# Performance work log

Measured on AMD Instinct MI355X. Metric: run time of the kernel, lower is better.

The kernel has to match this reference:

```python
import jax, jax.numpy as jnp
import numpy as np

B, S, HID = 1, 4096, 2048
NH, NKV, HD = 16, 4, 128
BLK, LOCAL, GNB, STRIDE = 64, 4, 2, 4
ROT = 64  # head_dim * rope_partial_rotary_factor(0.5), already even
SCALE = HD ** -0.5
NEG = -1e9


def _block_select(nb):
    """Static local+global key-block selection per query block (mirrors _select_key_blocks)."""
    sels = []
    for bi in range(nb):
        local = list(range(max(0, bi - LOCAL + 1), bi + 1))
        gc = list(range(0, bi + 1, STRIDE))
        if len(gc) > GNB:
            gc = gc[-GNB:]
        if 0 not in gc:
            gc = [0] + gc
        idx = sorted(set(local + gc))
        sels.append([i for i in idx if 0 <= i < nb and i <= bi])
    m = max(len(s) for s in sels)
    idx = np.zeros((nb, m), np.int32)
    valid = np.zeros((nb, m), bool)
    for i, s in enumerate(sels):
        idx[i, :len(s)] = s
        valid[i, :len(s)] = True
    return jnp.asarray(idx), jnp.asarray(valid)


def _rot_half(x):
    h = x.shape[-1] // 2
    return jnp.concatenate([-x[..., h:], x[..., :h]], axis=-1)


def setup_inputs() -> dict:
    key = jax.random.key(0)
    ks = jax.random.split(key, 8)
    w = lambda k, shp: (jax.random.normal(k, shp, jnp.float32) * 0.02)
    return {
        "hidden": jax.random.normal(ks[0], (B, S, HID), jnp.float32),
        "cos": jax.random.uniform(ks[1], (B, S, ROT), jnp.float32, -1.0, 1.0),
        "sin": jax.random.uniform(ks[2], (B, S, ROT), jnp.float32, -1.0, 1.0),
        "Wq": w(ks[3], (HID, NH * HD)),
        "Wk": w(ks[4], (HID, NKV * HD)),
        "Wv": w(ks[5], (HID, NKV * HD)),
        "Wo": w(ks[6], (NH * HD, HID)),
        "attn_mask": jnp.ones((B, S), jnp.float32),
    }


def reference(hidden, cos, sin, Wq, Wk, Wv, Wo, attn_mask):
    b_, s_, _ = hidden.shape
    q = (hidden @ Wq).reshape(b_, s_, NH, HD).transpose(0, 2, 1, 3)   # [B,H,S,d]
    k = (hidden @ Wk).reshape(b_, s_, NKV, HD).transpose(0, 2, 1, 3)  # [B,Hkv,S,d]
    v = (hidden @ Wv).reshape(b_, s_, NKV, HD).transpose(0, 2, 1, 3)

    # partial RoPE on first ROT channels
    c = cos[:, None, :, :]
    sn = sin[:, None, :, :]
    q1, q2 = q[..., :ROT], q[..., ROT:]
    k1, k2 = k[..., :ROT], k[..., ROT:]
    q = jnp.concatenate([q1 * c + _rot_half(q1) * sn, q2], axis=-1)
    k = jnp.concatenate([k1 * c + _rot_half(k1) * sn, k2], axis=-1)

    # repeat_kv (GQA expand: each kv head repeated contiguously)
    rep = NH // NKV
    k = jnp.repeat(k, rep, axis=1)
    v = jnp.repeat(v, rep, axis=1)

    nb = s_ // BLK  # S chosen divisible by BLK (pad_len == 0)
    qb = q.reshape(b_, NH, nb, BLK, HD)
    kb = k.reshape(b_, NH, nb, BLK, HD)
    vb = v.reshape(b_, NH, nb, BLK, HD)

    idx, valid = _block_select(nb)  # [nb, M]
    m = idx.shape[1]
    ksel = kb[:, :, idx]  # [B,H,nb,M,BLK,d]
    vsel = vb[:, :, idx]

    scores = jnp.einsum('bhnqd,bhnmkd->bhnqmk',
                        qb.astype(jnp.float32), ksel.astype(jnp.float32)) * SCALE
    # key-validity (padding) mask, additive as in original
    key_valid = attn_mask.reshape(b_, nb, BLK)
    kvm = key_valid[:, idx]  # [B,nb,M,BLK]
    scores = scores + (1.0 - kvm[:, None, :, None, :, :]) * NEG
    # invalid (padded) selected slots
    scores = jnp.where(valid[None, None, :, None, :, None], scores, NEG)
    # intra-block causal mask on the diagonal block
    intra = jnp.triu(jnp.ones((BLK, BLK), bool), 1)                    # [q,k]
    same = idx == jnp.arange(nb)[:, None]                              # [nb,M]
    diag = same[:, None, :, None] & intra[None, :, None, :]            # [nb,q,M,k]
    scores = jnp.where(diag[None, None], NEG, scores)

    probs = jax.nn.softmax(scores.reshape(b_, NH, nb, BLK, m * BLK), axis=-1)
    vflat = vsel.reshape(b_, NH, nb, m * BLK, HD)
    out = jnp.einsum('bhnqe,bhned->bhnqd', probs.astype(v.dtype), vflat)
    out = out.reshape(b_, NH, s_, HD).transpose(0, 2, 1, 3).reshape(b_, s_, NH * HD)
    return out @ Wo
```

## Files before the change

### kernel.cpp

```cpp
#include <hip/hip_runtime.h>
#include <hip/hip_bf16.h>


typedef short short8 __attribute__((ext_vector_type(8)));
typedef float f32x4  __attribute__((ext_vector_type(4)));

#define NEGV   (-1.0e9f)
#define SCALE  (0.08838834764831845f)

__device__ __forceinline__ void gload16(const void* g, void* l) {
  __builtin_amdgcn_global_load_lds(
      (const __attribute__((address_space(1))) unsigned int*)g,
      (__attribute__((address_space(3))) unsigned int*)l, 16, 0, 0);
}

__device__ __forceinline__ float bf2f(short s) {
  union { unsigned u; float f; } c;
  c.u = ((unsigned)(unsigned short)s) << 16;
  return c.f;
}

__device__ __forceinline__ short f2bf_s(float f) {
  __hip_bfloat16 b = __float2bfloat16(f);
  short s;
  __builtin_memcpy(&s, &b, 2);
  return s;
}

__global__ void conv_hidden(const float* __restrict__ H, __hip_bfloat16* __restrict__ X) {
  size_t t = (size_t)blockIdx.x * 256 + threadIdx.x;
  float4 v = *(const float4*)(H + t * 4);
  __hip_bfloat16* o = X + t * 4;
  o[0] = __float2bfloat16(v.x); o[1] = __float2bfloat16(v.y);
  o[2] = __float2bfloat16(v.z); o[3] = __float2bfloat16(v.w);
}

__global__ void transpose_f32_to_bf16(const float* __restrict__ src,
                                      __hip_bfloat16* __restrict__ dst,
                                      int R, int C) {
  __shared__ __hip_bfloat16 tile[64][73];
  int r0 = blockIdx.x * 64, c0 = blockIdx.y * 64;
  int c = threadIdx.x & 63, rq = threadIdx.x >> 6;
#pragma unroll
  for (int i = 0; i < 16; ++i) {
    int r = i * 4 + rq;
    tile[r][c] = __float2bfloat16(src[(size_t)(r0 + r) * C + c0 + c]);
  }
  __syncthreads();
#pragma unroll
  for (int i = 0; i < 16; ++i) {
    int cc = i * 4 + rq;
    dst[(size_t)(c0 + cc) * R + r0 + c] = tile[c][cc];
  }
}

__global__ void transpose_v(const __hip_bfloat16* __restrict__ Vb,
                            __hip_bfloat16* __restrict__ Vt) {
  __shared__ __hip_bfloat16 tile[64][73];
  int s0 = blockIdx.x * 64, c0 = blockIdx.y * 64;
  int c = threadIdx.x & 63, rq = threadIdx.x >> 6;
#pragma unroll
  for (int i = 0; i < 16; ++i) {
    int r = i * 4 + rq;
    tile[r][c] = Vb[(size_t)(s0 + r) * 512 + c0 + c];
  }
  __syncthreads();
#pragma unroll
  for (int i = 0; i < 16; ++i) {
    int cc = i * 4 + rq;
    Vt[(size_t)(c0 + cc) * 4096 + s0 + c] = tile[c][cc];
  }
}

__global__ void rope_inplace(const float* __restrict__ cosb, const float* __restrict__ sinb,
                             __hip_bfloat16* __restrict__ Qb, __hip_bfloat16* __restrict__ Kb) {
  int t = blockIdx.x * 256 + threadIdx.x;
  __hip_bfloat16* p;
  int s;
  if (t < 262144) {
    s = t >> 6;
    int rem = t & 63;
    p = Qb + (size_t)s * 2048 + (rem >> 2) * 128 + (rem & 3) * 8;
  } else {
    int tk = t - 262144;
    s = tk >> 4;
    int rem = tk & 15;
    p = Kb + (size_t)s * 512 + (rem >> 2) * 128 + (rem & 3) * 8;
  }
  const int g8 = (t & 3) * 8;
  const float* cp = cosb + (size_t)s * 64 + g8;
  const float* sp = sinb + (size_t)s * 64 + g8;
  short8 a = *(const short8*)p;
  short8 b = *(const short8*)(p + 32);
  float ca[8], sa[8], cb[8], sb[8];
  *(float4*)&ca[0] = *(const float4*)cp;        *(float4*)&ca[4] = *(const float4*)(cp + 4);
  *(float4*)&cb[0] = *(const float4*)(cp + 32); *(float4*)&cb[4] = *(const float4*)(cp + 36);
  *(float4*)&sa[0] = *(const float4*)sp;        *(float4*)&sa[4] = *(const float4*)(sp + 4);
  *(float4*)&sb[0] = *(const float4*)(sp + 32); *(float4*)&sb[4] = *(const float4*)(sp + 36);
  short8 oa, ob;
#pragma unroll
  for (int i = 0; i < 8; ++i) {
    float av = bf2f(a[i]), bv = bf2f(b[i]);
    oa[i] = f2bf_s(av * ca[i] - bv * sa[i]);
    ob[i] = f2bf_s(bv * cb[i] + av * sb[i]);
  }
  *(short8*)p = oa;
  *(short8*)(p + 32) = ob;
}

__global__ __launch_bounds__(512) void gemm_qkv256(
    const __hip_bfloat16* __restrict__ A, const __hip_bfloat16* __restrict__ Bt,
    __hip_bfloat16* __restrict__ Qb, __hip_bfloat16* __restrict__ Kb,
    __hip_bfloat16* __restrict__ Vb) {
  const int K = 2048;
  const int tid = threadIdx.x;
  const int wave = tid >> 6, lane = tid & 63;
  const int l15 = lane & 15, lg = lane >> 4;
  const int bm = blockIdx.x, bn = blockIdx.y;
  const int wm = wave >> 2, wn = wave & 3;

  __shared__ __hip_bfloat16 lds[2][32768];

  f32x4 acc[8][4] = {};
  const int lrow = lane >> 3;
  const int lslot = lane & 7;
  const size_t abase = (size_t)bm * 256 * K;
  const size_t bbase = (size_t)bn * 256 * K;
  const int r3 = l15 & 7;

#define STAGE_TILE(buf, k0)                                                        \
  do {                                                                             \
    _Pragma("unroll")                                                              \
    for (int c = 0; c < 4; ++c) {                                                  \
      int seg = c * 8 + wave;                                                      \
      int row = seg * 8 + lrow;                                                    \
      int col = (lslot ^ (row & 7)) * 8;                                           \
      gload16(A + abase + (size_t)row * K + (k0) + col, &lds[buf][seg * 512]);     \
      gload16(Bt + bbase + (size_t)row * K + (k0) + col, &lds[buf][16384 + seg * 512]); \
    }                                                                              \
  } while (0)

  STAGE_TILE(0, 0);

  for (int t = 0; t < 32; ++t) {
    asm volatile("s_waitcnt vmcnt(0)" ::: "memory");
    __builtin_amdgcn_s_barrier();
    __builtin_amdgcn_sched_barrier(0);
    if (t + 1 < 32) {
      const int nb = (t + 1) & 1;
      if (nb) STAGE_TILE(1, (t + 1) * 64); else STAGE_TILE(0, (t + 1) * 64);
    }
    const __hip_bfloat16* As_ = lds[t & 1];
    const __hip_bfloat16* Bs_ = lds[t & 1] + 16384;
#pragma unroll
    for (int kk = 0; kk < 2; ++kk) {
      const int slot = (kk * 4 + lg) ^ r3;
      short8 bf[4];
#pragma unroll
      for (int ni = 0; ni < 4; ++ni)
        bf[ni] = *(const short8*)&Bs_[(wn * 64 + ni * 16 + l15) * 64 + slot * 8];
#pragma unroll
      for (int mh = 0; mh < 2; ++mh) {
        short8 af[4];
#pragma unroll
        for (int mi = 0; mi < 4; ++mi)
          af[mi] = *(const short8*)&As_[(wm * 128 + mh * 64 + mi * 16 + l15) * 64 + slot * 8];
        __builtin_amdgcn_s_setprio(1);
#pragma unroll
        for (int mi = 0; mi < 4; ++mi)
#pragma unroll
          for (int ni = 0; ni < 4; ++ni)
            acc[mh * 4 + mi][ni] =
                __builtin_amdgcn_mfma_f32_16x16x32_bf16(af[mi], bf[ni], acc[mh * 4 + mi][ni], 0, 0, 0);
        __builtin_amdgcn_s_setprio(0);
      }
    }
  }
#undef STAGE_TILE

  __hip_bfloat16* dst; int ldc, coff;
  if (bn < 8)       { dst = Qb; ldc = 2048; coff = bn * 256; }
  else if (bn < 10) { dst = Kb; ldc = 512;  coff = bn * 256 - 2048; }
  else              { dst = Vb; ldc = 512;  coff = bn * 256 - 2560; }
#pragma unroll
  for (int m8 = 0; m8 < 8; ++m8)
#pragma unroll
    for (int ni = 0; ni < 4; ++ni) {
      int row = bm * 256 + wm * 128 + m8 * 16 + lg * 4;
      int col = coff + wn * 64 + ni * 16 + l15;
#pragma unroll
      for (int r = 0; r < 4; ++r)
        dst[(size_t)(row + r) * ldc + col] = __float2bfloat16(acc[m8][ni][r]);
    }
}

__global__ __launch_bounds__(256) void gemm_bt(
    const __hip_bfloat16* __restrict__ A, const __hip_bfloat16* __restrict__ Bt,
    float* __restrict__ C, int M, int N, int K) {
  const int tid = threadIdx.x;
  const int wave = tid >> 6, lane = tid & 63;
  const int l15 = lane & 15, lg = lane >> 4;
  const int bm = blockIdx.x, bn = blockIdx.y;
  const int wm = wave >> 1, wn = wave & 1;

  __shared__ __hip_bfloat16 As[128 * 64];
  __shared__ __hip_bfloat16 Bs[128 * 64];

  f32x4 acc[4][4] = {};
  const int lrow = lane >> 3;
  const int lslot = lane & 7;
  const int scol = (lslot ^ lrow) * 8;
  const size_t abase = (size_t)bm * 128 * K;
  const size_t bbase = (size_t)bn * 128 * K;
  const int r3 = l15 & 7;

  for (int k0 = 0; k0 < K; k0 += 64) {
#pragma unroll
    for (int i = 0; i < 4; ++i) {
      int seg = i * 4 + wave;
      int row = seg * 8 + lrow;
      gload16(A + abase + (size_t)row * K + k0 + scol, &As[seg * 512]);
      gload16(Bt + bbase + (size_t)row * K + k0 + scol, &Bs[seg * 512]);
    }
    __syncthreads();
#pragma unroll
    for (int ks = 0; ks < 2; ++ks) {
      const int slot = (ks * 4 + lg) ^ r3;
      short8 af[4], bf[4];
#pragma unroll
      for (int mi = 0; mi < 4; ++mi)
        af[mi] = *(const short8*)&As[(wm * 64 + mi * 16 + l15) * 64 + slot * 8];
#pragma unroll
      for (int ni = 0; ni < 4; ++ni)
        bf[ni] = *(const short8*)&Bs[(wn * 64 + ni * 16 + l15) * 64 + slot * 8];
#pragma unroll
      for (int mi = 0; mi < 4; ++mi)
#pragma unroll
        for (int ni = 0; ni < 4; ++ni)
          acc[mi][ni] = __builtin_amdgcn_mfma_f32_16x16x32_bf16(af[mi], bf[ni], acc[mi][ni], 0, 0, 0);
    }
    __syncthreads();
  }
#pragma unroll
  for (int mi = 0; mi < 4; ++mi)
#pragma unroll
    for (int ni = 0; ni < 4; ++ni) {
      int row = bm * 128 + wm * 64 + mi * 16 + lg * 4;
      int col = bn * 128 + wn * 64 + ni * 16 + l15;
#pragma unroll
      for (int r = 0; r < 4; ++r)
        C[(size_t)(row + r) * N + col] = acc[mi][ni][r];
    }
}

__global__ __launch_bounds__(256, 2) void attn_kernel(
    const __hip_bfloat16* __restrict__ Qb,
    const __hip_bfloat16* __restrict__ Kb,
    const __hip_bfloat16* __restrict__ Vt,
    const float* __restrict__ amask,
    __hip_bfloat16* __restrict__ AO)
{
  const int bid = blockIdx.x;
  const int h = bid & 15;
  const int bi = bid >> 4;
  const int kvh = h >> 2;
  const int tid = threadIdx.x;
  const int wave = tid >> 6, lane = tid & 63;
  const int l15 = lane & 15, lg = lane >> 4;

  int sel[6]; int nsel = 0;
  {
    int gtop = bi >> 2;
    for (int j = 0; j <= bi; ++j) {
      bool pick = (j == 0) || (j >= bi - 3) || (((j & 3) == 0) && ((j >> 2) >= gtop - 1));
      if (pick && nsel < 6) sel[nsel++] = j;
    }
  }

  __shared__ __hip_bfloat16 kvs[128 * 72];
  __shared__ __hip_bfloat16 Pb[64 * 72];

  short8 qf[4];
  {
    const __hip_bfloat16* qbase =
        Qb + (size_t)(bi * 64 + wave * 16 + l15) * 2048 + h * 128 + lg * 8;
#pragma unroll
    for (int ks = 0; ks < 4; ++ks) qf[ks] = *(const short8*)(qbase + ks * 32);
  }

  f32x4 sc[6][4] = {};
#pragma unroll
  for (int j = 0; j < 6; ++j) {
    if (j < nsel) {
      int kb = sel[j];
#pragma unroll
      for (int i = 0; i < 4; ++i) {
        int e = (i * 256 + tid) * 8;
        int r = e >> 7, c = e & 127;
        short8 v = *(const short8*)(Kb + (size_t)(kb * 64 + r) * 512 + kvh * 128 + c);
        *(short8*)&kvs[r * 136 + c] = v;
      }
      __syncthreads();
#pragma unroll
      for (int nf = 0; nf < 4; ++nf)
#pragma unroll
        for (int ks = 0; ks < 4; ++ks) {
          short8 bfr = *(const short8*)&kvs[(nf * 16 + l15) * 136 + ks * 32 + lg * 8];
          sc[j][nf] = __builtin_amdgcn_mfma_f32_16x16x32_bf16(qf[ks], bfr, sc[j][nf], 0, 0, 0);
        }
      __syncthreads();
    }
  }

  float rowmax[4] = {-3.0e38f, -3.0e38f, -3.0e38f, -3.0e38f};
#pragma unroll
  for (int j = 0; j < 6; ++j) {
    if (j >= nsel) continue;
    int kb = sel[j];
#pragma unroll
    for (int nf = 0; nf < 4; ++nf) {
      int keyg = kb * 64 + nf * 16 + l15;
      float mterm = (1.0f - amask[keyg]) * NEGV;
      int keyl = nf * 16 + l15;
#pragma unroll
      for (int r = 0; r < 4; ++r) {
        float s = sc[j][nf][r] * SCALE + mterm;
        if (kb == bi) {
          int qrow = wave * 16 + lg * 4 + r;
          if (keyl > qrow) s = NEGV;
        }
        sc[j][nf][r] = s;
        rowmax[r] = fmaxf(rowmax[r], s);
      }
    }
  }
#pragma unroll
  for (int r = 0; r < 4; ++r) {
    float v = rowmax[r];
    v = fmaxf(v, __shfl_xor(v, 1)); v = fmaxf(v, __shfl_xor(v, 2));
    v = fmaxf(v, __shfl_xor(v, 4)); v = fmaxf(v, __shfl_xor(v, 8));
    rowmax[r] = v;
  }
  float rinv[4] = {0.f, 0.f, 0.f, 0.f};
#pragma unroll
  for (int j = 0; j < 6; ++j) {
    if (j >= nsel) continue;
#pragma unroll
    for (int nf = 0; nf < 4; ++nf)
#pragma unroll
      for (int r = 0; r < 4; ++r) {
        float p = __expf(sc[j][nf][r] - rowmax[r]);
        sc[j][nf][r] = p;
        rinv[r] += p;
      }
  }
#pragma unroll
  for (int r = 0; r < 4; ++r) {
    float v = rinv[r];
    v += __shfl_xor(v, 1); v += __shfl_xor(v, 2);
    v += __shfl_xor(v, 4); v += __shfl_xor(v, 8);
    rinv[r] = 1.0f / v;
  }

  f32x4 oacc[8] = {};
#pragma unroll
  for (int j = 0; j < 6; ++j) {
    if (j < nsel) {
      int kb = sel[j];
#pragma unroll
      for (int nf = 0; nf < 4; ++nf)
#pragma unroll
        for (int r = 0; r < 4; ++r) {
          int qrow = wave * 16 + lg * 4 + r;
          Pb[qrow * 72 + nf * 16 + l15] = __float2bfloat16(sc[j][nf][r] * rinv[r]);
        }
#pragma unroll
      for (int i = 0; i < 4; ++i) {
        int e = (i * 256 + tid) * 8;
        int d = e >> 6, c = e & 63;
        short8 v = *(const short8*)(Vt + (size_t)(kvh * 128 + d) * 4096 + kb * 64 + c);
        *(short8*)&kvs[d * 72 + c] = v;
      }
      __syncthreads();
#pragma unroll
      for (int ks = 0; ks < 2; ++ks) {
        short8 pa = *(const short8*)&Pb[(wave * 16 + l15) * 72 + ks * 32 + lg * 8];
#pragma unroll
        for (int df = 0; df < 8; ++df) {
          short8 vb = *(const short8*)&kvs[(df * 16 + l15) * 72 + ks * 32 + lg * 8];
          oacc[df] = __builtin_amdgcn_mfma_f32_16x16x32_bf16(pa, vb, oacc[df], 0, 0, 0);
        }
      }
      __syncthreads();
    }
  }

#pragma unroll
  for (int df = 0; df < 8; ++df)
#pragma unroll
    for (int r = 0; r < 4; ++r) {
      int qrow = bi * 64 + wave * 16 + lg * 4 + r;
      AO[(size_t)qrow * 2048 + h * 128 + df * 16 + l15] = __float2bfloat16(oacc[df][r]);
    }
}

extern "C" void kernel_launch(void* const* d_in, const int* in_sizes, int n_in,
                              void* d_out, int out_size, void* d_ws, size_t ws_size,
                              hipStream_t stream) {
  const float* hidden = (const float*)d_in[0];
  const float* cosb   = (const float*)d_in[1];
  const float* sinb   = (const float*)d_in[2];
  const float* Wq     = (const float*)d_in[3];
  const float* Wk     = (const float*)d_in[4];
  const float* Wv     = (const float*)d_in[5];
  const float* Wo     = (const float*)d_in[6];
  const float* amask  = (const float*)d_in[7];

  char* ws = (char*)d_ws;
  __hip_bfloat16* Xb   = (__hip_bfloat16*)(ws);
  __hip_bfloat16* Wt   = (__hip_bfloat16*)(ws + 16777216);
  __hip_bfloat16* Wot  = (__hip_bfloat16*)(ws + 29360128);
  __hip_bfloat16* Qb   = (__hip_bfloat16*)(ws + 37748736);
  __hip_bfloat16* Kb   = (__hip_bfloat16*)(ws + 54525952);
  __hip_bfloat16* Vb   = (__hip_bfloat16*)(ws + 58720256);
  __hip_bfloat16* Vt   = (__hip_bfloat16*)(ws + 62914560);
  __hip_bfloat16* AO   = Xb;

  conv_hidden<<<8192, 256, 0, stream>>>(hidden, Xb);
  transpose_f32_to_bf16<<<dim3(32, 32), 256, 0, stream>>>(Wq, Wt, 2048, 2048);
  transpose_f32_to_bf16<<<dim3(32, 8),  256, 0, stream>>>(Wk, Wt + (size_t)2048 * 2048, 2048, 512);
  transpose_f32_to_bf16<<<dim3(32, 8),  256, 0, stream>>>(Wv, Wt + (size_t)2560 * 2048, 2048, 512);
  transpose_f32_to_bf16<<<dim3(32, 32), 256, 0, stream>>>(Wo, Wot, 2048, 2048);

  gemm_qkv256<<<dim3(16, 12), 512, 0, stream>>>(Xb, Wt, Qb, Kb, Vb);

  rope_inplace<<<1280, 256, 0, stream>>>(cosb, sinb, Qb, Kb);
  transpose_v<<<dim3(64, 8), 256, 0, stream>>>(Vb, Vt);

  attn_kernel<<<1024, 256, 0, stream>>>(Qb, Kb, Vt, amask, AO);

  gemm_bt<<<dim3(32, 16), 256, 0, stream>>>(AO, Wot, (float*)d_out, 4096, 2048, 2048);
}
```

Before: 174.8 us.

## Restructure QKV GEMM into eight-phase pipelined schedule with split half-tile loads

The QKV projection GEMM main loop is rewritten so each k-step runs four phases. In each phase a quarter of the A fragments is read from LDS and a half-tile of the next A or the B after that is issued as global-to-LDS loads, with barriers and partial vmcnt waits in between. B is prefetched two steps ahead and A one step ahead, which replaces the single full wait-and-barrier per iteration. This aims to spread memory traffic across the MFMA work and hide load latency. It adds more barriers per iteration, and a launch-bounds hint of two blocks per CU may constrain registers.

```diff
diff --git a/kernel.cpp b/kernel.cpp
--- a/kernel.cpp
+++ b/kernel.cpp
@@ -108,7 +108,7 @@
   *(short8*)(p + 32) = ob;
 }
 
-__global__ __launch_bounds__(512) void gemm_qkv256(
+__global__ __launch_bounds__(512, 2) void gemm_qkv8p(
     const __hip_bfloat16* __restrict__ A, const __hip_bfloat16* __restrict__ Bt,
     __hip_bfloat16* __restrict__ Qb, __hip_bfloat16* __restrict__ Kb,
     __hip_bfloat16* __restrict__ Vb) {
@@ -119,64 +119,90 @@
   const int bm = blockIdx.x, bn = blockIdx.y;
   const int wm = wave >> 2, wn = wave & 3;
 
-  __shared__ __hip_bfloat16 lds[2][32768];
+  __shared__ __hip_bfloat16 lds[65536];
 
   f32x4 acc[8][4] = {};
-  const int lrow = lane >> 3;
-  const int lslot = lane & 7;
+  const int srow = lane >> 3;
+  const int sslot = lane & 7;
+  const int scol = (sslot ^ srow) * 8;
   const size_t abase = (size_t)bm * 256 * K;
   const size_t bbase = (size_t)bn * 256 * K;
   const int r3 = l15 & 7;
 
-#define STAGE_TILE(buf, k0)                                                        \
-  do {                                                                             \
-    _Pragma("unroll")                                                              \
-    for (int c = 0; c < 4; ++c) {                                                  \
-      int seg = c * 8 + wave;                                                      \
-      int row = seg * 8 + lrow;                                                    \
-      int col = (lslot ^ (row & 7)) * 8;                                           \
-      gload16(A + abase + (size_t)row * K + (k0) + col, &lds[buf][seg * 512]);     \
-      gload16(Bt + bbase + (size_t)row * K + (k0) + col, &lds[buf][16384 + seg * 512]); \
-    }                                                                              \
+#define STAGE_HALF(SRC, SBASE, HALF, KO, LBASE)                                  \
+  do {                                                                           \
+    _Pragma("unroll")                                                            \
+    for (int l = 0; l < 2; ++l) {                                                \
+      int chunk = l * 8 + wave;                                                  \
+      int row = chunk * 8 + srow;                                                \
+      gload16(SRC + (SBASE) + (size_t)((HALF) * 128 + row) * K + (KO) + scol,    \
+              &lds[(LBASE) + chunk * 512]);                                      \
+    }                                                                            \
   } while (0)
 
-  STAGE_TILE(0, 0);
+  STAGE_HALF(Bt, bbase, 0, 0, 16384);
+  STAGE_HALF(Bt, bbase, 1, 0, 16384 + 8192);
+  STAGE_HALF(A, abase, 0, 0, 0);
+  STAGE_HALF(A, abase, 1, 0, 8192);
+  STAGE_HALF(Bt, bbase, 0, 64, 32768 + 16384);
+  STAGE_HALF(Bt, bbase, 1, 64, 32768 + 16384 + 8192);
+  asm volatile("s_waitcnt vmcnt(4)" ::: "memory");
+  __builtin_amdgcn_sched_barrier(0);
+  __builtin_amdgcn_s_barrier();
 
   for (int t = 0; t < 32; ++t) {
-    asm volatile("s_waitcnt vmcnt(0)" ::: "memory");
-    __builtin_amdgcn_s_barrier();
-    __builtin_amdgcn_sched_barrier(0);
-    if (t + 1 < 32) {
-      const int nb = (t + 1) & 1;
-      if (nb) STAGE_TILE(1, (t + 1) * 64); else STAGE_TILE(0, (t + 1) * 64);
-    }
-    const __hip_bfloat16* As_ = lds[t & 1];
-    const __hip_bfloat16* Bs_ = lds[t & 1] + 16384;
-#pragma unroll
-    for (int kk = 0; kk < 2; ++kk) {
-      const int slot = (kk * 4 + lg) ^ r3;
-      short8 bf[4];
-#pragma unroll
-      for (int ni = 0; ni < 4; ++ni)
-        bf[ni] = *(const short8*)&Bs_[(wn * 64 + ni * 16 + l15) * 64 + slot * 8];
-#pragma unroll
-      for (int mh = 0; mh < 2; ++mh) {
-        short8 af[4];
-#pragma unroll
-        for (int mi = 0; mi < 4; ++mi)
-          af[mi] = *(const short8*)&As_[(wm * 128 + mh * 64 + mi * 16 + l15) * 64 + slot * 8];
-        __builtin_amdgcn_s_setprio(1);
-#pragma unroll
-        for (int mi = 0; mi < 4; ++mi)
+    const int buf = (t & 1) * 32768;
+    const int nbuf = buf ^ 32768;
+    const int bA = buf + wm * 8192;
+    const int bB = buf + 16384 + (wn >> 1) * 8192;
+    short8 bfr[4][2];
+#pragma unroll
+    for (int q = 0; q < 4; ++q) {
+      if (q == 0) {
+#pragma unroll
+        for (int ni = 0; ni < 4; ++ni)
+#pragma unroll
+          for (int ks = 0; ks < 2; ++ks) {
+            int row = (wn & 1) * 64 + ni * 16 + l15;
+            int slot = (ks * 4 + lg) ^ r3;
+            bfr[ni][ks] = *(const short8*)&lds[bB + row * 64 + slot * 8];
+          }
+      }
+      short8 af[2][2];
+#pragma unroll
+      for (int m2 = 0; m2 < 2; ++m2)
+#pragma unroll
+        for (int ks = 0; ks < 2; ++ks) {
+          int row = (q * 2 + m2) * 16 + l15;
+          int slot = (ks * 4 + lg) ^ r3;
+          af[m2][ks] = *(const short8*)&lds[bA + row * 64 + slot * 8];
+        }
+      if (q == 0)      { if (t + 1 < 32) STAGE_HALF(A, abase, 0, (t + 1) * 64, nbuf); }
+      else if (q == 1) { if (t + 1 < 32) STAGE_HALF(A, abase, 1, (t + 1) * 64, nbuf + 8192); }
+      else if (q == 2) { if (t + 2 < 32) STAGE_HALF(Bt, bbase, 0, (t + 2) * 64, buf + 16384); }
+      else {
+        if (t + 2 < 32) STAGE_HALF(Bt, bbase, 1, (t + 2) * 64, buf + 16384 + 8192);
+        if (t < 30) asm volatile("s_waitcnt vmcnt(4)" ::: "memory");
+        else        asm volatile("s_waitcnt vmcnt(0)" ::: "memory");
+        __builtin_amdgcn_sched_barrier(0);
+      }
+      __builtin_amdgcn_s_barrier();
+      asm volatile("s_waitcnt lgkmcnt(0)" ::: "memory");
+      __builtin_amdgcn_sched_barrier(0);
+      __builtin_amdgcn_s_setprio(1);
+#pragma unroll
+      for (int ks = 0; ks < 2; ++ks)
+#pragma unroll
+        for (int m2 = 0; m2 < 2; ++m2)
 #pragma unroll
           for (int ni = 0; ni < 4; ++ni)
-            acc[mh * 4 + mi][ni] =
-                __builtin_amdgcn_mfma_f32_16x16x32_bf16(af[mi], bf[ni], acc[mh * 4 + mi][ni], 0, 0, 0);
-        __builtin_amdgcn_s_setprio(0);
-      }
-    }
-  }
-#undef STAGE_TILE
+            acc[q * 2 + m2][ni] = __builtin_amdgcn_mfma_f32_16x16x32_bf16(
+                af[m2][ks], bfr[ni][ks], acc[q * 2 + m2][ni], 0, 0, 0);
+      __builtin_amdgcn_s_setprio(0);
+      __builtin_amdgcn_s_barrier();
+    }
+  }
+#undef STAGE_HALF
 
   __hip_bfloat16* dst; int ldc, coff;
   if (bn < 8)       { dst = Qb; ldc = 2048; coff = bn * 256; }
@@ -432,7 +458,7 @@
   transpose_f32_to_bf16<<<dim3(32, 8),  256, 0, stream>>>(Wv, Wt + (size_t)2560 * 2048, 2048, 512);
   transpose_f32_to_bf16<<<dim3(32, 32), 256, 0, stream>>>(Wo, Wot, 2048, 2048);
 
-  gemm_qkv256<<<dim3(16, 12), 512, 0, stream>>>(Xb, Wt, Qb, Kb, Vb);
+  gemm_qkv8p<<<dim3(16, 12), 512, 0, stream>>>(Xb, Wt, Qb, Kb, Vb);
 
   rope_inplace<<<1280, 256, 0, stream>>>(cosb, sinb, Qb, Kb);
   transpose_v<<<dim3(64, 8), 256, 0, stream>>>(Vb, Vt);
```

New measurement: 176.8 us. Within noise of the previous version (+1.1%).
